# Performance work log

Measured on AMD Instinct MI355X. Metric: run time of the kernel, lower is better.

Reference implementation:

```python
import jax, jax.numpy as jnp
import numpy as np

B, T, C, H, N_LAYER, LAYER_ID = 4, 4096, 1024, 16, 12, 1
N = C // H  # head size = 64
EPS_LN = 1e-5
EPS_GN = 1e-5 * 64


def setup_inputs() -> dict:
    key = jax.random.key(0)
    ks = jax.random.split(key, 10)
    s = 0.02  # GPT-style init scale for linear weights
    W = lambda k, shp: (jax.random.normal(k, shp, jnp.float32) * s)
    # deterministic RWKV init formulas (torch.no_grad() block)
    ddd = np.arange(C, dtype=np.float64) / C
    r01 = LAYER_ID / (N_LAYER - 1)
    r1a0 = 1.0 - LAYER_ID / N_LAYER
    hh = np.arange(H, dtype=np.float64)
    inp = dict(
        x=jax.random.normal(ks[0], (B, T, C), jnp.float32),
        ln1_w=jnp.ones((C,), jnp.float32), ln1_b=jnp.zeros((C,), jnp.float32),
        tm_maa_k=jnp.asarray(1.0 - ddd ** r1a0, jnp.float32),
        tm_maa_v=jnp.asarray(1.0 - (ddd ** r1a0 + 0.3 * r01), jnp.float32),
        tm_maa_r=jnp.asarray(1.0 - ddd ** (0.5 * r1a0), jnp.float32),
        tm_maa_g=jnp.asarray(1.0 - ddd ** (0.5 * r1a0), jnp.float32),
        tm_decay=jnp.asarray(-6.0 + 5.0 * (hh / (H - 1)) ** (0.7 + 1.3 * r01), jnp.float32),
        tm_faaaa=jnp.asarray(r01 * (1.0 - hh / (H - 1)), jnp.float32),
        Wr=W(ks[1], (C, C)), Wk=W(ks[2], (C, C)), Wv=W(ks[3], (C, C)),
        Wg=W(ks[4], (C, C)), Wo=W(ks[5], (C, C)),
        gn_w=jnp.ones((C,), jnp.float32), gn_b=jnp.zeros((C,), jnp.float32),
        ln2_w=jnp.ones((C,), jnp.float32), ln2_b=jnp.zeros((C,), jnp.float32),
        cm_maa_k=jnp.asarray(1.0 - ddd ** r1a0, jnp.float32),
        cm_maa_r=jnp.asarray(1.0 - ddd ** r1a0, jnp.float32),
        Wck=W(ks[6], (3 * C, C)), Wcv=W(ks[7], (C, 3 * C)), Wcr=W(ks[8], (C, C)),
    )
    return inp


def _layernorm(x, w, b):
    mu = x.mean(-1, keepdims=True)
    var = ((x - mu) ** 2).mean(-1, keepdims=True)
    return (x - mu) * jax.lax.rsqrt(var + EPS_LN) * w + b


def _time_shift(x):  # ZeroPad2d((0,0,1,-1)): shift right by one step in time
    return jnp.concatenate([jnp.zeros_like(x[:, :1]), x[:, :-1]], axis=1)


def _time_mix(x, maa_k, maa_v, maa_r, maa_g, decay, faaaa, Wr, Wk, Wv, Wg, Wo, gn_w, gn_b):
    xx = _time_shift(x) - x
    xk = x + xx * maa_k
    xv = x + xx * maa_v
    xr = x + xx * maa_r
    xg = x + xx * maa_g
    r = (xr @ Wr.T).reshape(B, T, H, N).transpose(0, 2, 1, 3)   # B H T N
    k = (xk @ Wk.T).reshape(B, T, H, N).transpose(0, 2, 3, 1)   # B H N T
    v = (xv @ Wv.T).reshape(B, T, H, N).transpose(0, 2, 1, 3)   # B H T N
    g = jax.nn.silu(xg @ Wg.T)                                   # B T C
    Q = 256 if T % 256 == 0 else (128 if T % 128 == 0 else T)
    w = jnp.exp(-jnp.exp(decay))                                 # (H,)
    u = faaaa                                                    # (H,)
    ws = (w ** Q).reshape(1, H, 1, 1)
    wk = (w[:, None] ** jnp.arange(Q - 1, -1, -1)[None, :]).reshape(1, H, 1, Q)
    wb = (w[:, None] ** jnp.arange(Q)[None, :]).reshape(1, H, Q, 1)
    # intra-chunk decay matrix: W[i,j] = w^(i-j-1) if i>j, u if i==j, 0 if i<j
    ii = jnp.arange(Q)[:, None]
    jj = jnp.arange(Q)[None, :]
    e = jnp.clip(ii - jj - 1, 0, None)
    Wm = jnp.where(ii > jj, w[:, None, None] ** e[None], 0.0)
    Wm = jnp.where((ii == jj)[None], u[:, None, None], Wm)[None]  # (1,H,Q,Q)
    nc = T // Q
    rr = r.reshape(B, H, nc, Q, N).transpose(2, 0, 1, 3, 4)      # nc B H Q N
    kk = k.reshape(B, H, N, nc, Q).transpose(3, 0, 1, 2, 4)      # nc B H N Q
    vv = v.reshape(B, H, nc, Q, N).transpose(2, 0, 1, 3, 4)      # nc B H Q N

    def step(state, inp):
        rc, kc, vc = inp
        a = rc @ kc                                              # B H Q Q
        y = (a * Wm) @ vc + (rc @ state) * wb                    # B H Q N
        state = ws * state + (kc * wk) @ vc                      # B H N N
        return state, y

    state0 = jnp.zeros((B, H, N, N), x.dtype)
    _, ys = jax.lax.scan(step, state0, (rr, kk, vv))
    y = ys.transpose(1, 3, 0 + 2, 0, 4) if False else ys.transpose(1, 2, 0, 3, 4).reshape(B, H, T, N)
    y = y.transpose(0, 2, 1, 3)                                  # B T H N
    # GroupNorm(H groups over C), eps = 1e-5*64
    mu = y.mean(-1, keepdims=True)
    var = ((y - mu) ** 2).mean(-1, keepdims=True)
    y = ((y - mu) * jax.lax.rsqrt(var + EPS_GN)).reshape(B, T, C) * gn_w + gn_b
    return (y * g) @ Wo.T


def _channel_mix(x, maa_k, maa_r, Wck, Wcv, Wcr):
    xx = _time_shift(x) - x
    xk = x + xx * maa_k
    xr = x + xx * maa_r
    h = jnp.square(jax.nn.relu(xk @ Wck.T))   # B T 3C
    return jax.nn.sigmoid(xr @ Wcr.T) * (h @ Wcv.T)


def reference(x, ln1_w, ln1_b, tm_maa_k, tm_maa_v, tm_maa_r, tm_maa_g, tm_decay, tm_faaaa,
              Wr, Wk, Wv, Wg, Wo, gn_w, gn_b, ln2_w, ln2_b, cm_maa_k, cm_maa_r, Wck, Wcv, Wcr):
    x = x + _time_mix(_layernorm(x, ln1_w, ln1_b), tm_maa_k, tm_maa_v, tm_maa_r, tm_maa_g,
                      tm_decay, tm_faaaa, Wr, Wk, Wv, Wg, Wo, gn_w, gn_b)
    x = x + _channel_mix(_layernorm(x, ln2_w, ln2_b), cm_maa_k, cm_maa_r, Wck, Wcv, Wcr)
    return x
```

## Files before the change

kernel.cpp:

```cpp
#include <hip/hip_runtime.h>
#include <stdint.h>

constexpr int kB  = 4;
constexpr int kT  = 4096;
constexpr int kC  = 1024;
constexpr int kH  = 16;
constexpr int kN  = 64;
constexpr int kQ  = 256;
constexpr int kNC = 16;
constexpr int kBT = kB * kT;

typedef unsigned short u16;
typedef short  s16x8 __attribute__((ext_vector_type(8)));
typedef float  f32x4 __attribute__((ext_vector_type(4)));
typedef unsigned int __attribute__((address_space(1))) u32_as1;
typedef unsigned int __attribute__((address_space(3))) u32_as3;

struct U16x4 { u16 a, b, c, d; } __attribute__((aligned(8)));

__device__ __forceinline__ float bf2f(u16 h) {
  union { unsigned int u; float f; } v; v.u = ((unsigned int)h) << 16; return v.f;
}
__device__ __forceinline__ u16 f2bf(float f) {
  union { float f; unsigned int u; } v; v.f = f;
  unsigned int r = (v.u + 0x7FFFu + ((v.u >> 16) & 1u)) >> 16;
  return (u16)r;
}
__device__ __forceinline__ f32x4 mfma16(s16x8 a, s16x8 b, f32x4 c) {
  return __builtin_amdgcn_mfma_f32_16x16x32_bf16(a, b, c, 0, 0, 0);
}
__device__ __forceinline__ void gld16(const void* g, void* l) {
  __builtin_amdgcn_global_load_lds((const u32_as1*)g, (u32_as3*)l, 16, 0, 0);
}

struct WPtrs { const float* src[12]; };

__global__ __launch_bounds__(256)
void wconv_kernel(WPtrs p, u16* __restrict__ dst) {
  int chunk = blockIdx.y;
  const float* s = p.src[chunk];
  u16* d = dst + (size_t)chunk * (kC * kC);
  int idx = (blockIdx.x * 256 + threadIdx.x) * 4;
  float4 v = *(const float4*)&s[idx];
  U16x4 o = { f2bf(v.x), f2bf(v.y), f2bf(v.z), f2bf(v.w) };
  *(U16x4*)&d[idx] = o;
}

template<int NOUT>
__global__ __launch_bounds__(256)
void ln_mix_kernel(const float* __restrict__ x,
                   const float* __restrict__ lw, const float* __restrict__ lb,
                   const float* __restrict__ m0p, const float* __restrict__ m1p,
                   const float* __restrict__ m2p, const float* __restrict__ m3p,
                   u16* __restrict__ o0, u16* __restrict__ o1,
                   u16* __restrict__ o2, u16* __restrict__ o3)
{
  int row = blockIdx.x;
  int t = row & (kT - 1);
  int tid = threadIdx.x;
  int c0 = tid * 4;
  float4 xc = *(const float4*)&x[(size_t)row * kC + c0];
  float4 xp; xp.x = 0.f; xp.y = 0.f; xp.z = 0.f; xp.w = 0.f;
  bool hasprev = (t != 0);
  if (hasprev) xp = *(const float4*)&x[(size_t)(row - 1) * kC + c0];

  float s0 = xc.x + xc.y + xc.z + xc.w;
  float q0 = xc.x*xc.x + xc.y*xc.y + xc.z*xc.z + xc.w*xc.w;
  float s1 = xp.x + xp.y + xp.z + xp.w;
  float q1 = xp.x*xp.x + xp.y*xp.y + xp.z*xp.z + xp.w*xp.w;
  #pragma unroll
  for (int off = 1; off < 64; off <<= 1) {
    s0 += __shfl_xor(s0, off); q0 += __shfl_xor(q0, off);
    s1 += __shfl_xor(s1, off); q1 += __shfl_xor(q1, off);
  }
  __shared__ float red[16];
  int wid = tid >> 6, lane = tid & 63;
  if (lane == 0) { red[wid*4+0]=s0; red[wid*4+1]=q0; red[wid*4+2]=s1; red[wid*4+3]=q1; }
  __syncthreads();
  s0 = red[0]+red[4]+red[8]+red[12];
  q0 = red[1]+red[5]+red[9]+red[13];
  s1 = red[2]+red[6]+red[10]+red[14];
  q1 = red[3]+red[7]+red[11]+red[15];
  float mu0 = s0 * (1.f/kC), v0 = q0*(1.f/kC) - mu0*mu0, rs0 = rsqrtf(v0 + 1e-5f);
  float mu1 = s1 * (1.f/kC), v1 = q1*(1.f/kC) - mu1*mu1, rs1 = rsqrtf(v1 + 1e-5f);

  float cx[4] = { xc.x, xc.y, xc.z, xc.w };
  float px[4] = { xp.x, xp.y, xp.z, xp.w };
  U16x4 w0, w1, w2, w3;
  u16* p0 = (u16*)&w0; u16* p1 = (u16*)&w1; u16* p2 = (u16*)&w2; u16* p3 = (u16*)&w3;
  #pragma unroll
  for (int j = 0; j < 4; ++j) {
    int c = c0 + j;
    float lwc = lw[c], lbc = lb[c];
    float lnc = (cx[j] - mu0) * rs0 * lwc + lbc;
    float lnp = hasprev ? (px[j] - mu1) * rs1 * lwc + lbc : 0.f;
    float d = lnp - lnc;
    p0[j] = f2bf(lnc + d * m0p[c]);
    if (NOUT >= 2) p1[j] = f2bf(lnc + d * m1p[c]);
    if (NOUT >= 4) { p2[j] = f2bf(lnc + d * m2p[c]); p3[j] = f2bf(lnc + d * m3p[c]); }
  }
  size_t ob = (size_t)row * kC + c0;
  *(U16x4*)&o0[ob] = w0;
  if (NOUT >= 2) *(U16x4*)&o1[ob] = w1;
  if (NOUT >= 4) { *(U16x4*)&o2[ob] = w2; *(U16x4*)&o3[ob] = w3; }
}

enum { EPI_BF16 = 0, EPI_RESID = 1, EPI_RELU2 = 2, EPI_SIGMOID = 3,
       EPI_FINAL0 = 4, EPI_FINALACC = 5 };

#define GPHASE(p, mh, nh, bfv)                                                \
  {                                                                           \
    s16x8 afr[4][2], bfr[2][2];                                               \
    _Pragma("unroll") for (int mf = 0; mf < 4; ++mf)                          \
      _Pragma("unroll") for (int ks = 0; ks < 2; ++ks)                        \
        afr[mf][ks] = *(const s16x8*)&As[bfv][mh][                            \
            (wm2*64 + mf*16 + lo)*64 + 8*((ks*4 + q) ^ (lo & 7))];            \
    _Pragma("unroll") for (int nf = 0; nf < 2; ++nf)                          \
      _Pragma("unroll") for (int ks = 0; ks < 2; ++ks)                        \
        bfr[nf][ks] = *(const s16x8*)&Bs[bfv][nh][                            \
            (wn2*32 + nf*16 + lo)*64 + 8*((ks*4 + q) ^ (lo & 7))];            \
    __builtin_amdgcn_s_setprio(1);                                            \
    _Pragma("unroll") for (int mf = 0; mf < 4; ++mf)                          \
      _Pragma("unroll") for (int nf = 0; nf < 2; ++nf)                        \
        _Pragma("unroll") for (int ks = 0; ks < 2; ++ks)                      \
          acc[p][mf][nf] = mfma16(afr[mf][ks], bfr[nf][ks], acc[p][mf][nf]);  \
    __builtin_amdgcn_s_setprio(0);                                            \
  }

#define GWAIT(n) asm volatile("s_waitcnt vmcnt(" #n ")" ::: "memory")

template<int EPI, int LDB>
__global__ __launch_bounds__(512, 2)
void gemm256(const u16* __restrict__ A, const u16* __restrict__ Wt,
             void* __restrict__ out, const float* __restrict__ resid,
             const u16* __restrict__ sigb)
{
  constexpr int kKdim = 1024, kNdim = 1024, kLda = 1024;
  constexpr int NT = kKdim / 64;
  __shared__ u16 As[2][2][128 * 64];
  __shared__ u16 Bs[2][2][128 * 64];

  const int tid = threadIdx.x;
  const int w = tid >> 6, lane = tid & 63;
  const int lo = lane & 15, q = lane >> 4;
  const int wm2 = w >> 2, wn2 = w & 3;
  const int m0 = blockIdx.y * 256, n0 = blockIdx.x * 256;

  const int srow = lane >> 3;
  const int sch  = (lane & 7) ^ srow;

  const u16* Ag = A  + (size_t)m0 * kLda;
  const u16* Bg = Wt + (size_t)n0 * LDB;

  f32x4 acc[4][4][2] = {};

  auto stageA = [&](int bf, int kt, int h) {
    const u16* src = Ag + (size_t)(h*128 + w*8 + srow) * kLda + kt*64 + 8*sch;
    u16* dst = &As[bf][h][(w*8) * 64];
    gld16(src, dst);
    gld16(src + (size_t)64 * kLda, dst + 64*64);
  };
  auto stageB = [&](int bf, int kt, int h) {
    const u16* src = Bg + (size_t)(h*128 + w*8 + srow) * LDB + kt*64 + 8*sch;
    u16* dst = &Bs[bf][h][(w*8) * 64];
    gld16(src, dst);
    gld16(src + (size_t)64 * LDB, dst + 64*64);
  };

  stageA(0, 0, 0); stageB(0, 0, 0); stageB(0, 0, 1); stageA(0, 0, 1);

  for (int t = 0; t < NT - 1; ++t) {
    int bf = t & 1, nb = bf ^ 1;
    GWAIT(4);
    __builtin_amdgcn_s_barrier();
    stageA(nb, t + 1, 0);
    GPHASE(0, 0, 0, bf)
    GWAIT(4);
    __builtin_amdgcn_s_barrier();
    stageB(nb, t + 1, 0);
    GPHASE(1, 0, 1, bf)
    GWAIT(4);
    __builtin_amdgcn_s_barrier();
    stageB(nb, t + 1, 1);
    GPHASE(2, 1, 1, bf)
    stageA(nb, t + 1, 1);
    GPHASE(3, 1, 0, bf)
  }
  {
    constexpr int bf = (NT - 1) & 1;
    GWAIT(4);
    __builtin_amdgcn_s_barrier();
    GPHASE(0, 0, 0, bf)
    GWAIT(2);
    __builtin_amdgcn_s_barrier();
    GPHASE(1, 0, 1, bf)
    GWAIT(0);
    __builtin_amdgcn_s_barrier();
    GPHASE(2, 1, 1, bf)
    GPHASE(3, 1, 0, bf)
  }

  constexpr int MHq[4] = {0, 0, 1, 1}, NHq[4] = {0, 1, 1, 0};
  #pragma unroll
  for (int p = 0; p < 4; ++p) {
    #pragma unroll
    for (int mf = 0; mf < 4; ++mf) {
      #pragma unroll
      for (int nf = 0; nf < 2; ++nf) {
        #pragma unroll
        for (int rg = 0; rg < 4; ++rg) {
          int row = m0 + MHq[p]*128 + wm2*64 + mf*16 + q*4 + rg;
          int col = n0 + NHq[p]*128 + wn2*32 + nf*16 + lo;
          size_t idx = (size_t)row * kNdim + col;
          float v = acc[p][mf][nf][rg];
          if (EPI == EPI_BF16) {
            ((u16*)out)[idx] = f2bf(v);
          } else if (EPI == EPI_RESID) {
            ((float*)out)[idx] = resid[idx] + v;
          } else if (EPI == EPI_RELU2) {
            float tv = v > 0.f ? v : 0.f;
            ((u16*)out)[idx] = f2bf(tv * tv);
          } else if (EPI == EPI_SIGMOID) {
            ((u16*)out)[idx] = f2bf(1.f / (1.f + __expf(-v)));
          } else if (EPI == EPI_FINAL0) {
            float s = bf2f(sigb[idx]);
            ((float*)out)[idx] = resid[idx] + s * v;
          } else {
            float s = bf2f(sigb[idx]);
            ((float*)out)[idx] += s * v;
          }
        }
      }
    }
  }
}

template<bool DECAY>
__global__ __launch_bounds__(256)
void transpose_nt(const u16* __restrict__ src, const float* __restrict__ decay,
                  u16* __restrict__ dst)
{
  __shared__ u16 tile[64][72];
  int t0 = blockIdx.x * 64;
  int h  = blockIdx.y;
  int b  = blockIdx.z;
  int tid = threadIdx.x;
  int lrow = tid >> 3;
  int lcol = (tid & 7) * 8;
  float ed = DECAY ? __expf(decay[h]) : 0.f;

  #pragma unroll
  for (int rr = 0; rr < 2; ++rr) {
    int tr = lrow + rr * 32;
    *(uint4*)&tile[tr][lcol] =
        *(const uint4*)&src[((size_t)(b*kT + t0 + tr)) * kC + h*64 + lcol];
  }
  __syncthreads();
  #pragma unroll
  for (int rr = 0; rr < 2; ++rr) {
    int n = lrow + rr * 32;
    u16 o[8] __attribute__((aligned(16)));
    #pragma unroll
    for (int j = 0; j < 8; ++j) {
      int tglob = t0 + lcol + j;
      float v = bf2f(tile[lcol + j][n]);
      if (DECAY) v *= __expf(-ed * (float)(kQ - 1 - (tglob & (kQ - 1))));
      o[j] = f2bf(v);
    }
    *(uint4*)&dst[((size_t)((b*kH + h)*64 + n)) * kT + t0 + lcol] = *(uint4*)o;
  }
}

__global__ __launch_bounds__(256)
void sstate_kernel(const u16* __restrict__ kTw, const u16* __restrict__ vT,
                   const float* __restrict__ decay, u16* __restrict__ SinitT)
{
  __shared__ u16 kls[64 * 136];
  __shared__ u16 vls[64 * 136];
  int bh = blockIdx.x;
  int h = bh & (kH - 1);
  int tid = threadIdx.x, w = tid >> 6, lane = tid & 63;
  int lo = lane & 15, q = lane >> 4;
  float ed = __expf(decay[h]);
  float wQ = __expf(-ed * (float)kQ);
  const u16* kg = kTw + (size_t)bh * 64 * kT;
  const u16* vg = vT  + (size_t)bh * 64 * kT;
  f32x4 st[4] = {};
  for (int c = 0; c < kNC; ++c) {
    u16* ob = SinitT + ((size_t)bh * kNC + c) * 4096;
    #pragma unroll
    for (int nt = 0; nt < 4; ++nt)
      #pragma unroll
      for (int rg = 0; rg < 4; ++rg)
        ob[(w*16 + q*4 + rg) * 64 + nt*16 + lo] = f2bf(st[nt][rg]);
    f32x4 acc[4] = {};
    for (int half = 0; half < 2; ++half) {
      __syncthreads();
      #pragma unroll
      for (int it = 0; it < 4; ++it) {
        int row = it*16 + (tid >> 4);
        int c8  = (tid & 15) * 8;
        size_t gcol = (size_t)c * kQ + half*128 + c8;
        *(uint4*)&kls[row*136 + c8] = *(const uint4*)&kg[(size_t)row * kT + gcol];
        *(uint4*)&vls[row*136 + c8] = *(const uint4*)&vg[(size_t)row * kT + gcol];
      }
      __syncthreads();
      #pragma unroll
      for (int ks = 0; ks < 4; ++ks) {
        s16x8 av = *(const s16x8*)&vls[(w*16 + lo)*136 + ks*32 + q*8];
        #pragma unroll
        for (int nt = 0; nt < 4; ++nt) {
          s16x8 bv = *(const s16x8*)&kls[(nt*16 + lo)*136 + ks*32 + q*8];
          acc[nt] = mfma16(av, bv, acc[nt]);
        }
      }
    }
    #pragma unroll
    for (int nt = 0; nt < 4; ++nt) st[nt] = wQ * st[nt] + acc[nt];
  }
}

__global__ __launch_bounds__(256, 3)
void wkv_y_kernel(const u16* __restrict__ r, const u16* __restrict__ k,
                  const u16* __restrict__ vT, const u16* __restrict__ SinitT,
                  const u16* __restrict__ gpre, const float* __restrict__ decay,
                  const float* __restrict__ faaaa, const float* __restrict__ gnw,
                  const float* __restrict__ gnb, u16* __restrict__ yg)
{
  __shared__ u16 kls[2][64 * 64];
  __shared__ u16 vls[2][64 * 64];
  __shared__ u16 pbuf[64 * 72];
  __shared__ float wpow[kQ];

  int blk = blockIdx.x;
  int chunk = blk & (kNC - 1), bh = blk >> 4;
  int b = bh >> 4, h = bh & (kH - 1);
  int tid = threadIdx.x, w = tid >> 6, lane = tid & 63;
  int lo = lane & 15, q = lane >> 4;
  int t0 = chunk * kQ;
  float ed = __expf(decay[h]);
  wpow[tid] = __expf(-ed * (float)tid);
  float uu = faaaa[h];

  const size_t rbase = ((size_t)(b*kT + t0)) * kC + h*64;

  const int srow = lane >> 3;
  const int scol = 8 * ((lane & 7) ^ srow);
  const u16* kg0 = k  + ((size_t)(b*kT + t0)) * kC + h*64;
  const u16* vg0 = vT + ((size_t)(bh*64)) * kT + t0;

  auto stage = [&](int dstbuf, int jb_) {
    const u16* kgj = kg0 + (size_t)(jb_*64) * kC;
    const u16* vgj = vg0 + jb_*64;
    #pragma unroll
    for (int it = 0; it < 2; ++it) {
      int ci  = it*4 + w;
      int row = ci*8 + srow;
      gld16(kgj + (size_t)row * kC + scol, &kls[dstbuf][ci*512]);
      gld16(vgj + (size_t)row * kT + scol, &vls[dstbuf][ci*512]);
    }
  };

  stage(0, 0);

  s16x8 af[4][2];
  #pragma unroll
  for (int mt = 0; mt < 4; ++mt)
    #pragma unroll
    for (int ks = 0; ks < 2; ++ks)
      af[mt][ks] = *(const s16x8*)&r[rbase + (size_t)(mt*64 + w*16 + lo)*kC + ks*32 + q*8];

  f32x4 y[4][4] = {};
  {
    const u16* Sg = SinitT + (size_t)blk * 4096;
    #pragma unroll
    for (int ks = 0; ks < 2; ++ks) {
      s16x8 bf[4];
      #pragma unroll
      for (int nt = 0; nt < 4; ++nt)
        bf[nt] = *(const s16x8*)&Sg[(nt*16 + lo)*64 + ks*32 + q*8];
      #pragma unroll
      for (int mt = 0; mt < 4; ++mt)
        #pragma unroll
        for (int nt = 0; nt < 4; ++nt)
          y[mt][nt] = mfma16(af[mt][ks], bf[nt], y[mt][nt]);
    }
  }
  __syncthreads();

  #pragma unroll
  for (int mt = 0; mt < 4; ++mt)
    #pragma unroll
    for (int rg = 0; rg < 4; ++rg) {
      float wb = wpow[mt*64 + w*16 + q*4 + rg];
      #pragma unroll
      for (int nt = 0; nt < 4; ++nt) y[mt][nt][rg] *= wb;
    }

  u16* P = &pbuf[(w * 16) * 72];
  int buf = 0;
  #pragma unroll
  for (int jb = 0; jb < 4; ++jb) {
    if (jb < 3) stage(buf ^ 1, jb + 1);
    #pragma unroll
    for (int mt = jb; mt < 4; ++mt) {
      f32x4 a[4] = {};
      #pragma unroll
      for (int ks = 0; ks < 2; ++ks)
        #pragma unroll
        for (int nt = 0; nt < 4; ++nt) {
          s16x8 kf = *(const s16x8*)&kls[buf][(nt*16 + lo)*64 + 8*((ks*4 + q) ^ (lo & 7))];
          a[nt] = mfma16(af[mt][ks], kf, a[nt]);
        }
      #pragma unroll
      for (int nt = 0; nt < 4; ++nt)
        #pragma unroll
        for (int rg = 0; rg < 4; ++rg) {
          int i = mt*64 + w*16 + q*4 + rg;
          int j = jb*64 + nt*16 + lo;
          int d = i - j;
          float val = (d > 0) ? a[nt][rg] * wpow[d-1] : (d == 0 ? a[nt][rg] * uu : 0.f);
          P[(q*4 + rg)*72 + nt*16 + lo] = f2bf(val);
        }
      #pragma unroll
      for (int ks = 0; ks < 2; ++ks) {
        s16x8 pf = *(const s16x8*)&P[lo*72 + ks*32 + q*8];
        #pragma unroll
        for (int nt = 0; nt < 4; ++nt) {
          s16x8 vf = *(const s16x8*)&vls[buf][(nt*16 + lo)*64 + 8*((ks*4 + q) ^ (lo & 7))];
          y[mt][nt] = mfma16(pf, vf, y[mt][nt]);
        }
      }
    }
    __syncthreads();
    buf ^= 1;
  }

  float gw[4], gb[4];
  #pragma unroll
  for (int nt = 0; nt < 4; ++nt) {
    gw[nt] = gnw[h*64 + nt*16 + lo];
    gb[nt] = gnb[h*64 + nt*16 + lo];
  }
  for (int mt = 0; mt < 4; ++mt) {
    #pragma unroll
    for (int rg = 0; rg < 4; ++rg) {
      float s  = y[mt][0][rg] + y[mt][1][rg] + y[mt][2][rg] + y[mt][3][rg];
      float ss = y[mt][0][rg]*y[mt][0][rg] + y[mt][1][rg]*y[mt][1][rg]
               + y[mt][2][rg]*y[mt][2][rg] + y[mt][3][rg]*y[mt][3][rg];
      #pragma unroll
      for (int off = 1; off < 16; off <<= 1) {
        s  += __shfl_xor(s, off);
        ss += __shfl_xor(ss, off);
      }
      float mu  = s * (1.f/64.f);
      float var = ss * (1.f/64.f) - mu*mu;
      float rstd = rsqrtf(var + 6.4e-4f);
      #pragma unroll
      for (int nt = 0; nt < 4; ++nt) {
        float val = (y[mt][nt][rg] - mu) * rstd * gw[nt] + gb[nt];
        pbuf[(w*16 + q*4 + rg)*72 + nt*16 + lo] = f2bf(val);
      }
    }
    __syncthreads();
    #pragma unroll
    for (int it = 0; it < 2; ++it) {
      int lrow = it*32 + (tid >> 3);
      int c8  = (tid & 7) * 8;
      size_t ga = rbase + (size_t)(mt*64 + lrow)*kC + c8;
      uint2 ylo = *(const uint2*)&pbuf[lrow*72 + c8];
      uint2 yhi = *(const uint2*)&pbuf[lrow*72 + c8 + 4];
      uint4 gv = *(const uint4*)&gpre[ga];
      u16 yv[8] __attribute__((aligned(16)));
      const u16* ys = (const u16*)&ylo;
      const u16* gs = (const u16*)&gv;
      #pragma unroll
      for (int j = 0; j < 8; ++j) {
        u16 yj = (j < 4) ? ys[j] : ((const u16*)&yhi)[j-4];
        float g = bf2f(gs[j]);
        float sil = g / (1.f + __expf(-g));
        yv[j] = f2bf(bf2f(yj) * sil);
      }
      *(uint4*)&yg[ga] = *(uint4*)yv;
    }
    __syncthreads();
  }
}

extern "C" void kernel_launch(void* const* d_in, const int* in_sizes, int n_in,
                              void* d_out, int out_size, void* d_ws, size_t ws_size,
                              hipStream_t stream) {
  const size_t MB = 1024ull * 1024ull;
  if (ws_size < 192 * MB) return;

  const float* x     = (const float*)d_in[0];
  const float* ln1w  = (const float*)d_in[1];
  const float* ln1b  = (const float*)d_in[2];
  const float* tmk   = (const float*)d_in[3];
  const float* tmv   = (const float*)d_in[4];
  const float* tmr   = (const float*)d_in[5];
  const float* tmg   = (const float*)d_in[6];
  const float* decay = (const float*)d_in[7];
  const float* faaaa = (const float*)d_in[8];
  const float* Wr    = (const float*)d_in[9];
  const float* Wk    = (const float*)d_in[10];
  const float* Wv    = (const float*)d_in[11];
  const float* Wg    = (const float*)d_in[12];
  const float* Wo    = (const float*)d_in[13];
  const float* gnw   = (const float*)d_in[14];
  const float* gnb   = (const float*)d_in[15];
  const float* ln2w  = (const float*)d_in[16];
  const float* ln2b  = (const float*)d_in[17];
  const float* cmk   = (const float*)d_in[18];
  const float* cmr   = (const float*)d_in[19];
  const float* Wck   = (const float*)d_in[20];
  const float* Wcv   = (const float*)d_in[21];
  const float* Wcr   = (const float*)d_in[22];

  char* ws = (char*)d_ws;
  u16*   Wb     = (u16*)(ws +   0*MB);
  u16*   xr     = (u16*)(ws +  24*MB);
  u16*   xk     = (u16*)(ws +  56*MB);
  u16*   xv     = (u16*)(ws +  88*MB);
  u16*   xg     = (u16*)(ws + 120*MB);
  u16*   rb     = (u16*)(ws + 152*MB);
  u16*   kb     = (u16*)(ws +  24*MB);
  u16*   vb     = (u16*)(ws +  56*MB);
  u16*   gp     = (u16*)(ws +  88*MB);
  u16*   vT     = (u16*)(ws + 120*MB);
  u16*   kTw    = (u16*)(ws +  56*MB);
  u16*   SinitT = (u16*)(ws + 184*MB);
  u16*   yg     = (u16*)(ws +  56*MB);
  float* x1     = (float*)(ws + 88*MB);
  u16*   xck    = (u16*)(ws +  24*MB);
  u16*   xcr    = (u16*)(ws + 152*MB);
  u16*   sig    = (u16*)(ws +  56*MB);
  u16*   hbt    = (u16*)(ws + 152*MB);

  const int C2 = kC * kC;
  u16* Wr_b  = Wb + 0*(size_t)C2;
  u16* Wk_b  = Wb + 1*(size_t)C2;
  u16* Wv_b  = Wb + 2*(size_t)C2;
  u16* Wg_b  = Wb + 3*(size_t)C2;
  u16* Wo_b  = Wb + 4*(size_t)C2;
  u16* Wck_b = Wb + 5*(size_t)C2;
  u16* Wcv_b = Wb + 8*(size_t)C2;
  u16* Wcr_b = Wb + 11*(size_t)C2;

  WPtrs wp;
  wp.src[0] = Wr;  wp.src[1] = Wk;  wp.src[2] = Wv;  wp.src[3] = Wg;  wp.src[4] = Wo;
  wp.src[5] = Wck; wp.src[6] = Wck + C2; wp.src[7] = Wck + 2*(size_t)C2;
  wp.src[8] = Wcv; wp.src[9] = Wcv + C2; wp.src[10] = Wcv + 2*(size_t)C2;
  wp.src[11] = Wcr;
  wconv_kernel<<<dim3(C2/1024, 12), 256, 0, stream>>>(wp, Wb);

  ln_mix_kernel<4><<<kBT, 256, 0, stream>>>(x, ln1w, ln1b, tmr, tmk, tmv, tmg,
                                            xr, xk, xv, xg);
  gemm256<EPI_BF16, kC><<<dim3(4,64), 512, 0, stream>>>(xr, Wr_b, rb, nullptr, nullptr);
  gemm256<EPI_BF16, kC><<<dim3(4,64), 512, 0, stream>>>(xk, Wk_b, kb, nullptr, nullptr);
  gemm256<EPI_BF16, kC><<<dim3(4,64), 512, 0, stream>>>(xv, Wv_b, vb, nullptr, nullptr);
  gemm256<EPI_BF16, kC><<<dim3(4,64), 512, 0, stream>>>(xg, Wg_b, gp, nullptr, nullptr);

  transpose_nt<false><<<dim3(kT/64, kH, kB), 256, 0, stream>>>(vb, decay, vT);
  transpose_nt<true ><<<dim3(kT/64, kH, kB), 256, 0, stream>>>(kb, decay, kTw);
  sstate_kernel<<<kB*kH, 256, 0, stream>>>(kTw, vT, decay, SinitT);
  wkv_y_kernel<<<kB*kH*kNC, 256, 0, stream>>>(rb, kb, vT, SinitT, gp, decay, faaaa,
                                              gnw, gnb, yg);
  gemm256<EPI_RESID, kC><<<dim3(4,64), 512, 0, stream>>>(yg, Wo_b, x1, x, nullptr);

  ln_mix_kernel<2><<<kBT, 256, 0, stream>>>(x1, ln2w, ln2b, cmk, cmr, nullptr, nullptr,
                                            xck, xcr, nullptr, nullptr);
  gemm256<EPI_SIGMOID, kC><<<dim3(4,64), 512, 0, stream>>>(xcr, Wcr_b, sig, nullptr, nullptr);
  for (int i = 0; i < 3; ++i) {
    gemm256<EPI_RELU2, kC><<<dim3(4,64), 512, 0, stream>>>(
        xck, Wck_b + (size_t)i*C2, hbt, nullptr, nullptr);
    if (i == 0)
      gemm256<EPI_FINAL0, 3*kC><<<dim3(4,64), 512, 0, stream>>>(
          hbt, Wcv_b + (size_t)i*kC, (float*)d_out, x1, sig);
    else
      gemm256<EPI_FINALACC, 3*kC><<<dim3(4,64), 512, 0, stream>>>(
          hbt, Wcv_b + (size_t)i*kC, (float*)d_out, x1, sig);
  }
}
```

Before: 1.131 ms.

## Parallelize chunk-state computation, swizzle GEMM blocks, merge channel-mix GEMMs

The serial per-(b,h) state kernel is split into a chunk-parallel kernel that computes each chunk's k^T v contribution across 1024 blocks, followed by a light scan kernel that applies the decay recurrence. The GEMM gains a block-index swizzle that groups workgroups in strides of eight, intended to improve L2 locality. The three channel-mix value GEMMs, each with K=1024, are replaced by one GEMM with K=3072 over a stored full hidden buffer, which removes the two read-modify-write passes over the fp32 output. The x1 intermediate is written straight into the output buffer and accumulated in place, at the cost of a larger hidden workspace.

Measured after the change: 1.019 ms. -9.9%, faster.

```diff
diff --git a/kernel.cpp b/kernel.cpp
--- a/kernel.cpp
+++ b/kernel.cpp
@@ -129,14 +129,13 @@
 
 #define GWAIT(n) asm volatile("s_waitcnt vmcnt(" #n ")" ::: "memory")
 
-template<int EPI, int LDB>
+template<int EPI, int LDB, int KDIM = 1024, int LDC = 1024>
 __global__ __launch_bounds__(512, 2)
 void gemm256(const u16* __restrict__ A, const u16* __restrict__ Wt,
              void* __restrict__ out, const float* __restrict__ resid,
              const u16* __restrict__ sigb)
 {
-  constexpr int kKdim = 1024, kNdim = 1024, kLda = 1024;
-  constexpr int NT = kKdim / 64;
+  constexpr int NT = KDIM / 64;
   __shared__ u16 As[2][2][128 * 64];
   __shared__ u16 Bs[2][2][128 * 64];
 
@@ -144,21 +143,27 @@
   const int w = tid >> 6, lane = tid & 63;
   const int lo = lane & 15, q = lane >> 4;
   const int wm2 = w >> 2, wn2 = w & 3;
-  const int m0 = blockIdx.y * 256, n0 = blockIdx.x * 256;
+
+  const int nwg = gridDim.x * gridDim.y;
+  const int orig = blockIdx.y * gridDim.x + blockIdx.x;
+  const int cpx = nwg >> 3;
+  const int wg = (orig & 7) * cpx + (orig >> 3);
+  const int n0 = (wg % gridDim.x) * 256;
+  const int m0 = (wg / gridDim.x) * 256;
 
   const int srow = lane >> 3;
   const int sch  = (lane & 7) ^ srow;
 
-  const u16* Ag = A  + (size_t)m0 * kLda;
+  const u16* Ag = A  + (size_t)m0 * KDIM;
   const u16* Bg = Wt + (size_t)n0 * LDB;
 
   f32x4 acc[4][4][2] = {};
 
   auto stageA = [&](int bf, int kt, int h) {
-    const u16* src = Ag + (size_t)(h*128 + w*8 + srow) * kLda + kt*64 + 8*sch;
+    const u16* src = Ag + (size_t)(h*128 + w*8 + srow) * KDIM + kt*64 + 8*sch;
     u16* dst = &As[bf][h][(w*8) * 64];
     gld16(src, dst);
-    gld16(src + (size_t)64 * kLda, dst + 64*64);
+    gld16(src + (size_t)64 * KDIM, dst + 64*64);
   };
   auto stageB = [&](int bf, int kt, int h) {
     const u16* src = Bg + (size_t)(h*128 + w*8 + srow) * LDB + kt*64 + 8*sch;
@@ -211,7 +216,7 @@
         for (int rg = 0; rg < 4; ++rg) {
           int row = m0 + MHq[p]*128 + wm2*64 + mf*16 + q*4 + rg;
           int col = n0 + NHq[p]*128 + wn2*32 + nf*16 + lo;
-          size_t idx = (size_t)row * kNdim + col;
+          size_t idx = (size_t)row * LDC + col;
           float v = acc[p][mf][nf][rg];
           if (EPI == EPI_BF16) {
             ((u16*)out)[idx] = f2bf(v);
@@ -272,51 +277,70 @@
 }
 
 __global__ __launch_bounds__(256)
-void sstate_kernel(const u16* __restrict__ kTw, const u16* __restrict__ vT,
-                   const float* __restrict__ decay, u16* __restrict__ SinitT)
+void schunk_kernel(const u16* __restrict__ kTw, const u16* __restrict__ vT,
+                   u16* __restrict__ SinitT)
 {
   __shared__ u16 kls[64 * 136];
   __shared__ u16 vls[64 * 136];
+  int blk = blockIdx.x;
+  int c = blk & (kNC - 1), bh = blk >> 4;
+  int tid = threadIdx.x, w = tid >> 6, lane = tid & 63;
+  int lo = lane & 15, q = lane >> 4;
+  const u16* kg = kTw + (size_t)bh * 64 * kT;
+  const u16* vg = vT  + (size_t)bh * 64 * kT;
+  f32x4 acc[4] = {};
+  for (int half = 0; half < 2; ++half) {
+    __syncthreads();
+    #pragma unroll
+    for (int it = 0; it < 4; ++it) {
+      int row = it*16 + (tid >> 4);
+      int c8  = (tid & 15) * 8;
+      size_t gcol = (size_t)c * kQ + half*128 + c8;
+      *(uint4*)&kls[row*136 + c8] = *(const uint4*)&kg[(size_t)row * kT + gcol];
+      *(uint4*)&vls[row*136 + c8] = *(const uint4*)&vg[(size_t)row * kT + gcol];
+    }
+    __syncthreads();
+    #pragma unroll
+    for (int ks = 0; ks < 4; ++ks) {
+      s16x8 av = *(const s16x8*)&vls[(w*16 + lo)*136 + ks*32 + q*8];
+      #pragma unroll
+      for (int nt = 0; nt < 4; ++nt) {
+        s16x8 bv = *(const s16x8*)&kls[(nt*16 + lo)*136 + ks*32 + q*8];
+        acc[nt] = mfma16(av, bv, acc[nt]);
+      }
+    }
+  }
+  u16* ob = SinitT + ((size_t)bh * kNC + c) * 4096;
+  #pragma unroll
+  for (int nt = 0; nt < 4; ++nt)
+    #pragma unroll
+    for (int rg = 0; rg < 4; ++rg)
+      ob[(w*16 + q*4 + rg) * 64 + nt*16 + lo] = f2bf(acc[nt][rg]);
+}
+
+__global__ __launch_bounds__(256)
+void sscan_kernel(const float* __restrict__ decay, u16* __restrict__ SinitT)
+{
   int bh = blockIdx.x;
   int h = bh & (kH - 1);
-  int tid = threadIdx.x, w = tid >> 6, lane = tid & 63;
-  int lo = lane & 15, q = lane >> 4;
-  float ed = __expf(decay[h]);
-  float wQ = __expf(-ed * (float)kQ);
-  const u16* kg = kTw + (size_t)bh * 64 * kT;
-  const u16* vg = vT  + (size_t)bh * 64 * kT;
-  f32x4 st[4] = {};
+  float wQ = __expf(-__expf(decay[h]) * (float)kQ);
+  u16* base = SinitT + ((size_t)bh * kNC) * 4096 + threadIdx.x * 16;
+  float S[16];
+  #pragma unroll
+  for (int i = 0; i < 16; ++i) S[i] = 0.f;
   for (int c = 0; c < kNC; ++c) {
-    u16* ob = SinitT + ((size_t)bh * kNC + c) * 4096;
-    #pragma unroll
-    for (int nt = 0; nt < 4; ++nt)
-      #pragma unroll
-      for (int rg = 0; rg < 4; ++rg)
-        ob[(w*16 + q*4 + rg) * 64 + nt*16 + lo] = f2bf(st[nt][rg]);
-    f32x4 acc[4] = {};
-    for (int half = 0; half < 2; ++half) {
-      __syncthreads();
-      #pragma unroll
-      for (int it = 0; it < 4; ++it) {
-        int row = it*16 + (tid >> 4);
-        int c8  = (tid & 15) * 8;
-        size_t gcol = (size_t)c * kQ + half*128 + c8;
-        *(uint4*)&kls[row*136 + c8] = *(const uint4*)&kg[(size_t)row * kT + gcol];
-        *(uint4*)&vls[row*136 + c8] = *(const uint4*)&vg[(size_t)row * kT + gcol];
-      }
-      __syncthreads();
-      #pragma unroll
-      for (int ks = 0; ks < 4; ++ks) {
-        s16x8 av = *(const s16x8*)&vls[(w*16 + lo)*136 + ks*32 + q*8];
-        #pragma unroll
-        for (int nt = 0; nt < 4; ++nt) {
-          s16x8 bv = *(const s16x8*)&kls[(nt*16 + lo)*136 + ks*32 + q*8];
-          acc[nt] = mfma16(av, bv, acc[nt]);
-        }
-      }
-    }
-    #pragma unroll
-    for (int nt = 0; nt < 4; ++nt) st[nt] = wQ * st[nt] + acc[nt];
+    u16* p = base + (size_t)c * 4096;
+    u16 tmp[16] __attribute__((aligned(16)));
+    *(uint4*)&tmp[0] = *(const uint4*)p;
+    *(uint4*)&tmp[8] = *(const uint4*)(p + 8);
+    u16 outv[16] __attribute__((aligned(16)));
+    #pragma unroll
+    for (int i = 0; i < 16; ++i) {
+      outv[i] = f2bf(S[i]);
+      S[i] = wQ * S[i] + bf2f(tmp[i]);
+    }
+    *(uint4*)p = *(uint4*)&outv[0];
+    *(uint4*)(p + 8) = *(uint4*)&outv[8];
   }
 }
 
@@ -531,11 +555,10 @@
   u16*   kTw    = (u16*)(ws +  56*MB);
   u16*   SinitT = (u16*)(ws + 184*MB);
   u16*   yg     = (u16*)(ws +  56*MB);
-  float* x1     = (float*)(ws + 88*MB);
   u16*   xck    = (u16*)(ws +  24*MB);
   u16*   xcr    = (u16*)(ws + 152*MB);
   u16*   sig    = (u16*)(ws +  56*MB);
-  u16*   hbt    = (u16*)(ws + 152*MB);
+  u16*   hbt    = (u16*)(ws +  88*MB);
 
   const int C2 = kC * kC;
   u16* Wr_b  = Wb + 0*(size_t)C2;
@@ -563,22 +586,18 @@
 
   transpose_nt<false><<<dim3(kT/64, kH, kB), 256, 0, stream>>>(vb, decay, vT);
   transpose_nt<true ><<<dim3(kT/64, kH, kB), 256, 0, stream>>>(kb, decay, kTw);
-  sstate_kernel<<<kB*kH, 256, 0, stream>>>(kTw, vT, decay, SinitT);
+  schunk_kernel<<<kB*kH*kNC, 256, 0, stream>>>(kTw, vT, SinitT);
+  sscan_kernel<<<kB*kH, 256, 0, stream>>>(decay, SinitT);
   wkv_y_kernel<<<kB*kH*kNC, 256, 0, stream>>>(rb, kb, vT, SinitT, gp, decay, faaaa,
                                               gnw, gnb, yg);
-  gemm256<EPI_RESID, kC><<<dim3(4,64), 512, 0, stream>>>(yg, Wo_b, x1, x, nullptr);
-
-  ln_mix_kernel<2><<<kBT, 256, 0, stream>>>(x1, ln2w, ln2b, cmk, cmr, nullptr, nullptr,
-                                            xck, xcr, nullptr, nullptr);
+  gemm256<EPI_RESID, kC><<<dim3(4,64), 512, 0, stream>>>(yg, Wo_b, d_out, x, nullptr);
+
+  ln_mix_kernel<2><<<kBT, 256, 0, stream>>>((const float*)d_out, ln2w, ln2b, cmk, cmr,
+                                            nullptr, nullptr, xck, xcr, nullptr, nullptr);
   gemm256<EPI_SIGMOID, kC><<<dim3(4,64), 512, 0, stream>>>(xcr, Wcr_b, sig, nullptr, nullptr);
-  for (int i = 0; i < 3; ++i) {
-    gemm256<EPI_RELU2, kC><<<dim3(4,64), 512, 0, stream>>>(
-        xck, Wck_b + (size_t)i*C2, hbt, nullptr, nullptr);
-    if (i == 0)
-      gemm256<EPI_FINAL0, 3*kC><<<dim3(4,64), 512, 0, stream>>>(
-          hbt, Wcv_b + (size_t)i*kC, (float*)d_out, x1, sig);
-    else
-      gemm256<EPI_FINALACC, 3*kC><<<dim3(4,64), 512, 0, stream>>>(
-          hbt, Wcv_b + (size_t)i*kC, (float*)d_out, x1, sig);
-  }
-}
+  for (int i = 0; i < 3; ++i)
+    gemm256<EPI_RELU2, kC, 1024, 3*kC><<<dim3(4,64), 512, 0, stream>>>(
+        xck, Wck_b + (size_t)i*C2, hbt + (size_t)i*kC, nullptr, nullptr);
+  gemm256<EPI_FINALACC, 3*kC, 3*kC, kC><<<dim3(4,64), 512, 0, stream>>>(
+      hbt, Wcv_b, (float*)d_out, nullptr, sig);
+}
```
